# Kernel tuning notes

Hardware: AMD Instinct MI355X
Metric: run time of the kernel (lower is better)

Reference implementation:

```python
import jax, jax.numpy as jnp
import numpy as np

D_MODEL = 2048
DT_RANK = 64


def setup_inputs() -> dict:
    key = jax.random.key(0)
    ks = jax.random.split(key, 9)
    x = jax.random.normal(ks[0], (4, 2048, D_MODEL), dtype=jnp.float32)
    A = jax.random.normal(ks[1], (D_MODEL, D_MODEL), dtype=jnp.float32)
    B = jax.random.normal(ks[2], (D_MODEL, D_MODEL), dtype=jnp.float32)
    C = jax.random.normal(ks[3], (D_MODEL, D_MODEL), dtype=jnp.float32)
    Dp = jax.random.normal(ks[4], (1, D_MODEL), dtype=jnp.float32)
    # dt_project: Linear(d_model -> dt_rank); dt_project_out: Linear(dt_rank -> d_model)
    lim1 = 1.0 / np.sqrt(D_MODEL)
    W1 = jax.random.uniform(ks[5], (DT_RANK, D_MODEL), minval=-lim1, maxval=lim1, dtype=jnp.float32)
    b1 = jax.random.uniform(ks[6], (DT_RANK,), minval=-lim1, maxval=lim1, dtype=jnp.float32)
    lim2 = 1.0 / np.sqrt(DT_RANK)
    W2 = jax.random.uniform(ks[7], (D_MODEL, DT_RANK), minval=-lim2, maxval=lim2, dtype=jnp.float32)
    b2 = jax.random.uniform(ks[8], (D_MODEL,), minval=-lim2, maxval=lim2, dtype=jnp.float32)
    return {"x": x, "A": A, "B": B, "C": C, "Dp": Dp, "W1": W1, "b1": b1, "W2": W2, "b2": b2}


def reference(x, A, B, C, Dp, W1, b1, W2, b2):
    # dt = Linear_out(gelu(Linear_in(x)))  -- torch uses exact (erf) gelu
    h = jax.nn.gelu(jnp.einsum('bld,rd->blr', x, W1) + b1, approximate=False)
    dt = jnp.einsum('blr,dr->bld', h, W2) + b2
    # per-timestep loop collapses to one batched GEMM: x @ (A+B+C)
    out = jnp.einsum('bld,ds->bls', x, A + B + C)
    return out * dt + Dp  # Dp broadcasts (1, d_model)
```

## Files before the change

### kernel.cpp

```cpp
#include <hip/hip_runtime.h>
#include <stdint.h>

#define D 2048
#define R 64
#define M_TOTAL 8192

typedef float f32x4 __attribute__((ext_vector_type(4)));
typedef __bf16 bf16x8 __attribute__((ext_vector_type(8)));
typedef unsigned short u16x8 __attribute__((ext_vector_type(8)));
typedef unsigned short u16x4 __attribute__((ext_vector_type(4)));

__device__ __forceinline__ unsigned short f2bf(float f) {
  unsigned u = __builtin_bit_cast(unsigned, f);
  u += 0x7FFFu + ((u >> 16) & 1u);
  return (unsigned short)(u >> 16);
}

__device__ __forceinline__ u16x8 pack8(float4 a, float4 b) {
  u16x8 o = { f2bf(a.x), f2bf(a.y), f2bf(a.z), f2bf(a.w),
              f2bf(b.x), f2bf(b.y), f2bf(b.z), f2bf(b.w) };
  return o;
}

__device__ __forceinline__ void gload_lds16(const void* g, void* l) {
  __builtin_amdgcn_global_load_lds(
      (const __attribute__((address_space(1))) void*)g,
      (__attribute__((address_space(3))) void*)l, 16, 0, 0);
}

__device__ __forceinline__ void gload_lds_asm(const unsigned short* g, int lds_byte) {
  asm volatile("s_mov_b32 m0, %1\n\t"
               "global_load_lds_dwordx4 %0, off"
               :: "v"(g), "s"(lds_byte)
               : "memory");
}

__device__ __forceinline__ int lds_addr(const void* p) {
  return (int)(size_t)(const __attribute__((address_space(3))) void*)p;
}

__global__ __launch_bounds__(512) void prep_kernel(
    const float* __restrict__ x, const float* __restrict__ A,
    const float* __restrict__ B, const float* __restrict__ C,
    const float* __restrict__ w1, const float* __restrict__ b1,
    const float* __restrict__ w2,
    unsigned short* __restrict__ xbf, unsigned short* __restrict__ st,
    unsigned short* __restrict__ w2bf, unsigned short* __restrict__ hbf) {
  __shared__ unsigned short plds[24576];
  const int t = threadIdx.x;
  const int bx = blockIdx.x;

  if (bx < 256) {
    unsigned short* sX = plds;
    unsigned short* sW = plds + 8192;
    const int m0 = bx * 32;
    const int kq = t >> 7, u = t & 127;
    const int row = u >> 2, c = u & 3;
    const int row_w = u >> 1, cw0 = (u & 1) * 2;
    const float* xp = x + (size_t)(m0 + row) * D + kq * 512 + c * 8;
    const float* wp = w1 + (size_t)row_w * D + kq * 512 + cw0 * 8;
    unsigned short* xw = xbf + (size_t)(m0 + row) * D + kq * 512 + c * 8;
    unsigned short* sXw = sX + kq * 2048 + row * 32 + (c ^ ((row >> 1) & 3)) * 8;
    const int rw2 = (row_w >> 1) & 3;
    unsigned short* sWw0 = sW + kq * 4096 + row_w * 32 + (cw0 ^ rw2) * 8;
    unsigned short* sWw1 = sW + kq * 4096 + row_w * 32 + ((cw0 + 1) ^ rw2) * 8;
    const int w = t >> 6, l = t & 63, lm = l & 15, lk = l >> 4;
    const int kqw = w >> 1, rg = w & 1;
    const int rslot = (lk ^ ((lm >> 1) & 3)) * 8;
    const unsigned short* sXr = sX + kqw * 2048 + (rg * 16 + lm) * 32 + rslot;
    const unsigned short* sWr = sW + kqw * 4096 + lm * 32 + rslot;

    f32x4 acc[4] = {};
    float4 qx[2][2], qw[2][4];
#define HLOADX(P, KT) do { qx[P][0] = *(const float4*)(xp + (KT) * 32); \
                           qx[P][1] = *(const float4*)(xp + (KT) * 32 + 4); } while (0)
#define HLOADW(P, KT) do { qw[P][0] = *(const float4*)(wp + (KT) * 32); \
                           qw[P][1] = *(const float4*)(wp + (KT) * 32 + 4); \
                           qw[P][2] = *(const float4*)(wp + (KT) * 32 + 8); \
                           qw[P][3] = *(const float4*)(wp + (KT) * 32 + 12); } while (0)
    HLOADX(0, 0); HLOADW(0, 0); HLOADX(1, 1); HLOADW(1, 1);
#define HSTEP(P, KT) do { \
    u16x8 ox = pack8(qx[P][0], qx[P][1]); \
    *(u16x8*)(sXw + (P) * 1024) = ox; \
    *(u16x8*)(xw + (KT) * 32) = ox; \
    *(u16x8*)(sWw0 + (P) * 2048) = pack8(qw[P][0], qw[P][1]); \
    *(u16x8*)(sWw1 + (P) * 2048) = pack8(qw[P][2], qw[P][3]); \
    if ((KT) + 2 < 16) { HLOADX(P, (KT) + 2); HLOADW(P, (KT) + 2); } \
    __syncthreads(); \
    { bf16x8 a_ = __builtin_bit_cast(bf16x8, *(const u16x8*)(sXr + (P) * 1024)); \
      _Pragma("unroll") \
      for (int j = 0; j < 4; ++j) { \
        bf16x8 b_ = __builtin_bit_cast(bf16x8, *(const u16x8*)(sWr + (P) * 2048 + j * 512)); \
        acc[j] = __builtin_amdgcn_mfma_f32_16x16x32_bf16(a_, b_, acc[j], 0, 0, 0); \
      } } } while (0)
#pragma unroll 1
    for (int it = 0; it < 8; ++it) { HSTEP(0, it * 2); HSTEP(1, it * 2 + 1); }
#undef HSTEP
#undef HLOADX
#undef HLOADW

    __syncthreads();
    float* red = (float*)plds;
    if (kqw > 0) {
#pragma unroll
      for (int j = 0; j < 4; ++j)
        *(f32x4*)(red + (((((kqw - 1) * 2 + rg) * 4) + j) * 64 + l) * 4) = acc[j];
    }
    __syncthreads();
    if (kqw == 0) {
      int m_base = m0 + rg * 16 + lk * 4;
#pragma unroll
      for (int j = 0; j < 4; ++j) {
        f32x4 s = acc[j];
#pragma unroll
        for (int q = 1; q < 4; ++q)
          s += *(const f32x4*)(red + (((((q - 1) * 2 + rg) * 4) + j) * 64 + l) * 4);
        int n = j * 16 + lm;
        float bv = b1[n];
#pragma unroll
        for (int r = 0; r < 4; ++r) {
          float v = s[r] + bv;
          float g = 0.5f * v * (1.0f + erff(v * 0.70710678118654752f));
          hbf[(size_t)(m_base + r) * R + n] = f2bf(g);
        }
      }
    }
  } else if (bx < 768) {
    unsigned short (*lds)[68] = (unsigned short(*)[68])plds;
    const int id = bx - 256;
    const int k0 = (id >> 5) * 128, n0 = (id & 31) * 64;
#pragma unroll
    for (int q = 0; q < 4; ++q) {
      int rowq = q * 32 + (t >> 4);
      int col = (t & 15) * 4;
      size_t off = (size_t)(k0 + rowq) * D + n0 + col;
      float4 a = *(const float4*)(A + off);
      float4 b = *(const float4*)(B + off);
      float4 cc = *(const float4*)(C + off);
      u16x4 o = { f2bf(a.x + b.x + cc.x), f2bf(a.y + b.y + cc.y),
                  f2bf(a.z + b.z + cc.z), f2bf(a.w + b.w + cc.w) };
      *(u16x4*)(&lds[rowq][col]) = o;
    }
    __syncthreads();
    const int n = t >> 3, kc = (t & 7) * 16;
    u16x8 v0, v1;
#pragma unroll
    for (int jj = 0; jj < 8; ++jj) v0[jj] = lds[kc + jj][n];
#pragma unroll
    for (int jj = 0; jj < 8; ++jj) v1[jj] = lds[kc + 8 + jj][n];
    size_t ooff = (size_t)(n0 + n) * D + k0 + kc;
    *(u16x8*)(st + ooff) = v0;
    *(u16x8*)(st + ooff + 8) = v1;
  } else {
    const int NW4 = (D * R) / 4;
    for (int i = (bx - 768) * 512 + t; i < NW4; i += 4 * 512) {
      float4 v = ((const float4*)w2)[i];
      u16x4 o = { f2bf(v.x), f2bf(v.y), f2bf(v.z), f2bf(v.w) };
      *(u16x4*)(w2bf + (size_t)i * 4) = o;
    }
  }
}

__global__ __launch_bounds__(512, 2) void gemm_kernel(
    const unsigned short* __restrict__ xbf, const unsigned short* __restrict__ st,
    const unsigned short* __restrict__ hbf, const unsigned short* __restrict__ w2bf,
    const float* __restrict__ b2, const float* __restrict__ dp,
    float* __restrict__ out) {
  __shared__ unsigned short sA[4 * 8192];
  __shared__ unsigned short sB[4 * 8192];
  const int tid = threadIdx.x;
  const int w = tid >> 6, l = tid & 63, lk = l >> 4, lm = l & 15;
  const int wm = w >> 2, wn = w & 3;
  int bid = blockIdx.x;
  int wg = (bid & 7) * 32 + (bid >> 3);
  int mb = wg >> 3, nb = wg & 7;
  int m0 = mb * 256, n0 = nb * 256;

  const int kg = (tid & 3) ^ ((tid >> 2) & 3);
  const unsigned short* gA = xbf + (size_t)(m0 + (tid >> 2)) * D + kg * 8;
  const unsigned short* gB = st + (size_t)(n0 + (tid >> 2)) * D + kg * 8;
  const int sAb = __builtin_amdgcn_readfirstlane(lds_addr(sA) + w * 1024);
  const int sBb = __builtin_amdgcn_readfirstlane(lds_addr(sB) + w * 1024);

  const int gsw = (lk ^ (lm & 3)) * 8;
  const int arow = (wm * 128 + lm) * 32;
  const int brow = (wn * 64 + lm) * 32;

  const int NT = D / 32;
  f32x4 acc[8][4] = {};
  bf16x8 aE[8], bE[4], aO[8], bO[4];

#define LD8(buf, off) __builtin_bit_cast(bf16x8, *(const u16x8*)((buf) + (off)))
#define SB0() __builtin_amdgcn_sched_barrier(0)
#define BAR() __builtin_amdgcn_s_barrier()

#define STAGE_T(T) do { if ((T) < NT) { \
    const unsigned short* ga_ = gA + (T) * 32; \
    int la_ = sAb + ((T) & 3) * 16384; \
    gload_lds_asm(ga_, la_); \
    gload_lds_asm(ga_ + 128 * D, la_ + 8192); \
    const unsigned short* gb_ = gB + (T) * 32; \
    int lb_ = sBb + ((T) & 3) * 16384; \
    gload_lds_asm(gb_, lb_); \
    gload_lds_asm(gb_ + 128 * D, lb_ + 8192); } } while (0)

#define RD_T(S, AR, BR) do { \
    const unsigned short* bA_ = sA + (S) * 8192; \
    const unsigned short* bB_ = sB + (S) * 8192; \
    _Pragma("unroll") for (int i = 0; i < 8; ++i) \
      AR[i] = LD8(bA_, arow + i * 512 + gsw); \
    _Pragma("unroll") for (int j = 0; j < 4; ++j) \
      BR[j] = LD8(bB_, brow + j * 512 + gsw); } while (0)

#define MM32(AR, BR) do { \
    __builtin_amdgcn_s_setprio(1); \
    _Pragma("unroll") for (int i = 0; i < 8; ++i) \
    _Pragma("unroll") for (int j = 0; j < 4; ++j) \
      acc[i][j] = __builtin_amdgcn_mfma_f32_16x16x32_bf16(AR[i], BR[j], acc[i][j], 0, 0, 0); \
    __builtin_amdgcn_s_setprio(0); } while (0)

#define PHASE(KT, CA, CB, NA, NB) do { \
    RD_T(((KT) + 1) & 3, NA, NB); \
    STAGE_T((KT) + 3); \
    SB0(); \
    asm volatile("s_waitcnt lgkmcnt(12)" ::: "memory"); \
    SB0(); \
    MM32(CA, CB); \
    SB0(); \
    if ((KT) < NT - 3) asm volatile("s_waitcnt vmcnt(4)" ::: "memory"); \
    else               asm volatile("s_waitcnt vmcnt(0)" ::: "memory"); \
    SB0(); BAR(); } while (0)

  STAGE_T(0); STAGE_T(1); STAGE_T(2);
  asm volatile("s_waitcnt vmcnt(4)" ::: "memory");
  BAR();
  RD_T(0, aE, bE);
  SB0();

#pragma unroll 1
  for (int it = 0; it < NT / 2; ++it) {
    const int kt0 = it * 2;
    PHASE(kt0, aE, bE, aO, bO);
    PHASE(kt0 + 1, aO, bO, aE, bE);
  }

  bf16x8 wb0[4], wb1[4];
  float b2v[4], dpv[4];
#pragma unroll
  for (int j = 0; j < 4; ++j) {
    int n = n0 + wn * 64 + j * 16 + lm;
    const u16x8* wp = (const u16x8*)(w2bf + (size_t)n * R + lk * 8);
    wb0[j] = __builtin_bit_cast(bf16x8, wp[0]);
    wb1[j] = __builtin_bit_cast(bf16x8, wp[4]);
    b2v[j] = b2[n];
    dpv[j] = dp[n];
  }
#pragma unroll
  for (int mi = 0; mi < 8; ++mi) {
    int hrow = m0 + wm * 128 + mi * 16 + lm;
    const u16x8* hp = (const u16x8*)(hbf + (size_t)hrow * R + lk * 8);
    bf16x8 ha0 = __builtin_bit_cast(bf16x8, hp[0]);
    bf16x8 ha1 = __builtin_bit_cast(bf16x8, hp[4]);
    int mbase = m0 + wm * 128 + mi * 16 + lk * 4;
#pragma unroll
    for (int j = 0; j < 4; ++j) {
      f32x4 dt = {};
      dt = __builtin_amdgcn_mfma_f32_16x16x32_bf16(ha0, wb0[j], dt, 0, 0, 0);
      dt = __builtin_amdgcn_mfma_f32_16x16x32_bf16(ha1, wb1[j], dt, 0, 0, 0);
      int n = n0 + wn * 64 + j * 16 + lm;
#pragma unroll
      for (int r = 0; r < 4; ++r) {
        float val = acc[mi][j][r] * (dt[r] + b2v[j]) + dpv[j];
        out[(size_t)(mbase + r) * D + n] = val;
      }
    }
  }
#undef PHASE
#undef MM32
#undef RD_T
#undef STAGE_T
#undef BAR
#undef SB0
#undef LD8
}

extern "C" void kernel_launch(void* const* d_in, const int* in_sizes, int n_in,
                              void* d_out, int out_size, void* d_ws, size_t ws_size,
                              hipStream_t stream) {
  const float* x  = (const float*)d_in[0];
  const float* A  = (const float*)d_in[1];
  const float* B  = (const float*)d_in[2];
  const float* C  = (const float*)d_in[3];
  const float* Dp = (const float*)d_in[4];
  const float* W1 = (const float*)d_in[5];
  const float* b1 = (const float*)d_in[6];
  const float* W2 = (const float*)d_in[7];
  const float* b2 = (const float*)d_in[8];
  float* out = (float*)d_out;

  uint8_t* ws = (uint8_t*)d_ws;
  unsigned short* xbf  = (unsigned short*)ws;
  unsigned short* st   = (unsigned short*)(ws + (32u << 20));
  unsigned short* w2bf = (unsigned short*)(ws + (40u << 20));
  unsigned short* hbf  = (unsigned short*)(ws + (41u << 20));

  prep_kernel<<<772, 512, 0, stream>>>(x, A, B, C, W1, b1, W2, xbf, st, w2bf, hbf);
  gemm_kernel<<<256, 512, 0, stream>>>(xbf, st, hbf, w2bf, b2, Dp, out);
}
```

Measured before the change: 102.1 us.

## Load A operand directly from global into registers, stage only B in LDS

The GEMM main loop stops staging the x (A) tile through LDS. Each wave now loads its A fragments straight from global memory into registers one tile ahead, while B is still staged through LDS with a new swizzle pattern. This halves LDS traffic and capacity use and drops the A ds_reads. In exchange each wave issues many more global loads, and A rows are re-fetched by the different wn waves without any sharing, which relies on the cache. The wait counts and the LDS read order are also reworked.

```diff
diff --git a/kernel.cpp b/kernel.cpp
--- a/kernel.cpp
+++ b/kernel.cpp
@@ -20,12 +20,6 @@
   u16x8 o = { f2bf(a.x), f2bf(a.y), f2bf(a.z), f2bf(a.w),
               f2bf(b.x), f2bf(b.y), f2bf(b.z), f2bf(b.w) };
   return o;
-}
-
-__device__ __forceinline__ void gload_lds16(const void* g, void* l) {
-  __builtin_amdgcn_global_load_lds(
-      (const __attribute__((address_space(1))) void*)g,
-      (__attribute__((address_space(3))) void*)l, 16, 0, 0);
 }
 
 __device__ __forceinline__ void gload_lds_asm(const unsigned short* g, int lds_byte) {
@@ -34,7 +28,16 @@
                :: "v"(g), "s"(lds_byte)
                : "memory");
 }
-
+__device__ __forceinline__ u16x8 gload_b128(const unsigned short* p) {
+  u16x8 r;
+  asm volatile("global_load_dwordx4 %0, %1, off" : "=v"(r) : "v"(p) : "memory");
+  return r;
+}
+__device__ __forceinline__ u16x8 dsread_b128(int addr) {
+  u16x8 r;
+  asm volatile("ds_read_b128 %0, %1" : "=v"(r) : "v"(addr) : "memory");
+  return r;
+}
 __device__ __forceinline__ int lds_addr(const void* p) {
   return (int)(size_t)(const __attribute__((address_space(3))) void*)p;
 }
@@ -166,7 +169,6 @@
     const unsigned short* __restrict__ hbf, const unsigned short* __restrict__ w2bf,
     const float* __restrict__ b2, const float* __restrict__ dp,
     float* __restrict__ out) {
-  __shared__ unsigned short sA[4 * 8192];
   __shared__ unsigned short sB[4 * 8192];
   const int tid = threadIdx.x;
   const int w = tid >> 6, l = tid & 63, lk = l >> 4, lm = l & 15;
@@ -176,72 +178,63 @@
   int mb = wg >> 3, nb = wg & 7;
   int m0 = mb * 256, n0 = nb * 256;
 
-  const int kg = (tid & 3) ^ ((tid >> 2) & 3);
-  const unsigned short* gA = xbf + (size_t)(m0 + (tid >> 2)) * D + kg * 8;
-  const unsigned short* gB = st + (size_t)(n0 + (tid >> 2)) * D + kg * 8;
-  const int sAb = __builtin_amdgcn_readfirstlane(lds_addr(sA) + w * 1024);
+  const int kgB = (tid & 3) ^ ((tid >> 3) & 3);
+  const unsigned short* gB = st + (size_t)(n0 + (tid >> 2)) * D + kgB * 8;
   const int sBb = __builtin_amdgcn_readfirstlane(lds_addr(sB) + w * 1024);
 
-  const int gsw = (lk ^ (lm & 3)) * 8;
-  const int arow = (wm * 128 + lm) * 32;
-  const int brow = (wn * 64 + lm) * 32;
+  const int bAddr = lds_addr(sB) + (wn * 64 + lm) * 64 + ((lk ^ ((lm >> 1) & 3)) << 4);
+  const unsigned short* aBase = xbf + (size_t)(m0 + wm * 128 + lm) * D + lk * 8;
 
   const int NT = D / 32;
   f32x4 acc[8][4] = {};
-  bf16x8 aE[8], bE[4], aO[8], bO[4];
-
-#define LD8(buf, off) __builtin_bit_cast(bf16x8, *(const u16x8*)((buf) + (off)))
+  u16x8 aE[8], aO[8], bR[4];
+
 #define SB0() __builtin_amdgcn_sched_barrier(0)
 #define BAR() __builtin_amdgcn_s_barrier()
 
-#define STAGE_T(T) do { if ((T) < NT) { \
-    const unsigned short* ga_ = gA + (T) * 32; \
-    int la_ = sAb + ((T) & 3) * 16384; \
-    gload_lds_asm(ga_, la_); \
-    gload_lds_asm(ga_ + 128 * D, la_ + 8192); \
+#define STAGE_B(T) do { if ((T) < NT) { \
     const unsigned short* gb_ = gB + (T) * 32; \
-    int lb_ = sBb + ((T) & 3) * 16384; \
+    int lb_ = sBb + (((T) & 3) << 14); \
     gload_lds_asm(gb_, lb_); \
     gload_lds_asm(gb_ + 128 * D, lb_ + 8192); } } while (0)
 
-#define RD_T(S, AR, BR) do { \
-    const unsigned short* bA_ = sA + (S) * 8192; \
-    const unsigned short* bB_ = sB + (S) * 8192; \
-    _Pragma("unroll") for (int i = 0; i < 8; ++i) \
-      AR[i] = LD8(bA_, arow + i * 512 + gsw); \
-    _Pragma("unroll") for (int j = 0; j < 4; ++j) \
-      BR[j] = LD8(bB_, brow + j * 512 + gsw); } while (0)
-
-#define MM32(AR, BR) do { \
+#define LD_A(KT, AR) do { _Pragma("unroll") for (int i = 0; i < 8; ++i) \
+    AR[i] = gload_b128(aBase + (size_t)(i * 16) * D + (KT) * 32); } while (0)
+
+#define RD_B(S) do { _Pragma("unroll") for (int j = 0; j < 4; ++j) \
+    bR[j] = dsread_b128(bAddr + ((S) << 14) + j * 1024); } while (0)
+
+#define MM32(AR) do { \
     __builtin_amdgcn_s_setprio(1); \
     _Pragma("unroll") for (int i = 0; i < 8; ++i) \
     _Pragma("unroll") for (int j = 0; j < 4; ++j) \
-      acc[i][j] = __builtin_amdgcn_mfma_f32_16x16x32_bf16(AR[i], BR[j], acc[i][j], 0, 0, 0); \
+      acc[i][j] = __builtin_amdgcn_mfma_f32_16x16x32_bf16( \
+          __builtin_bit_cast(bf16x8, AR[i]), __builtin_bit_cast(bf16x8, bR[j]), \
+          acc[i][j], 0, 0, 0); \
     __builtin_amdgcn_s_setprio(0); } while (0)
 
-#define PHASE(KT, CA, CB, NA, NB) do { \
-    RD_T(((KT) + 1) & 3, NA, NB); \
-    STAGE_T((KT) + 3); \
+#define TILE(KT, CA, NA) do { \
+    LD_A((KT) + 1, NA); \
+    STAGE_B((KT) + 3); \
+    RD_B((KT) & 3); \
     SB0(); \
-    asm volatile("s_waitcnt lgkmcnt(12)" ::: "memory"); \
+    asm volatile("s_waitcnt lgkmcnt(0)" ::: "memory"); \
+    if ((KT) < NT - 4) asm volatile("s_waitcnt vmcnt(10)" ::: "memory"); \
+    else               asm volatile("s_waitcnt vmcnt(0)" ::: "memory"); \
     SB0(); \
-    MM32(CA, CB); \
-    SB0(); \
-    if ((KT) < NT - 3) asm volatile("s_waitcnt vmcnt(4)" ::: "memory"); \
-    else               asm volatile("s_waitcnt vmcnt(0)" ::: "memory"); \
+    MM32(CA); \
     SB0(); BAR(); } while (0)
 
-  STAGE_T(0); STAGE_T(1); STAGE_T(2);
-  asm volatile("s_waitcnt vmcnt(4)" ::: "memory");
+  STAGE_B(0); STAGE_B(1); STAGE_B(2);
+  LD_A(0, aE);
+  asm volatile("s_waitcnt vmcnt(12)" ::: "memory");
   BAR();
-  RD_T(0, aE, bE);
-  SB0();
 
 #pragma unroll 1
   for (int it = 0; it < NT / 2; ++it) {
     const int kt0 = it * 2;
-    PHASE(kt0, aE, bE, aO, bO);
-    PHASE(kt0 + 1, aO, bO, aE, bE);
+    TILE(kt0, aE, aO);
+    TILE(kt0 + 1, aO, aE);
   }
 
   bf16x8 wb0[4], wb1[4];
@@ -275,13 +268,13 @@
       }
     }
   }
-#undef PHASE
+#undef TILE
 #undef MM32
-#undef RD_T
-#undef STAGE_T
+#undef RD_B
+#undef LD_A
+#undef STAGE_B
 #undef BAR
 #undef SB0
-#undef LD8
 }
 
 extern "C" void kernel_launch(void* const* d_in, const int* in_sizes, int n_in,
```

New measurement: 173.8 us. +70.3%, slower.
